# Optimization experiments

Hardware: AMD Instinct MI355X
Metric: run time of the kernel (lower is better)

The kernel has to match this reference:

```python
import jax, jax.numpy as jnp
import numpy as np
from jax.scipy.linalg import expm

B = 16384
K = 64          # number of subgroups
M = 6           # mat_dim per subgroup (subgroup_size = 36)
NUM_ACTIONS = 16


def setup_inputs() -> dict:
    key = jax.random.key(0)
    k1, k2, k3, k4 = jax.random.split(key, 4)
    group_feats = jax.random.normal(k1, (B, K * M * M), dtype=jnp.float32)
    act = jax.random.randint(k2, (B,), 0, NUM_ACTIONS)
    act_params = jax.random.normal(k3, (NUM_ACTIONS, K), dtype=jnp.float32) * 0.001
    lie_alg_basis = jax.random.normal(k4, (K, M, M), dtype=jnp.float32)
    return {"group_feats": group_feats, "act": act,
            "act_params": act_params, "lie_alg_basis": lie_alg_basis}


def reference(group_feats, act, act_params, lie_alg_basis):
    # apply_act: act_repr = blockdiag_k expm(a_{bk} * (L_k - L_k^T)); out = act_repr @ blockdiag(group_feats)
    sel = act_params[act]                                   # [B, K]  (index_select on act_params)
    skew = lie_alg_basis - jnp.swapaxes(lie_alg_basis, -2, -1)  # [K, M, M]
    lie_alg = sel[:, :, None, None] * skew[None]            # [B, K, M, M]
    # batched matrix exponential over all B*K small blocks
    lie_group = jax.vmap(expm)(lie_alg.reshape(-1, M, M)).reshape(B, K, M, M)
    gf_mat = group_feats.reshape(B, K, M, M)                # to_group_matrix (block-diag blocks)
    # block-diagonal matmul == full dense matmul since off-diagonal blocks are zero
    post = jnp.einsum('bkij,bkjl->bkil', lie_group, gf_mat)
    return post.reshape(B, K * M * M)                       # to_group_feats
```

## Files before the change

### kernel.cpp

```cpp
#include <hip/hip_runtime.h>
#include <stdint.h>

#define BATCH 16384
#define KSUB 64
#define MDIM 6
#define MM 36
#define NACT 16
#define F4PB 9
#define BLK 256
#define LDSPITCH 37

__global__ void expm_table_kernel(const float* __restrict__ act_params,
                                  const float* __restrict__ basis,
                                  float* __restrict__ Rtab)
{
    int gid = blockIdx.x * blockDim.x + threadIdx.x;
    if (gid >= NACT * KSUB) return;
    int a = gid / KSUB;
    int k = gid - a * KSUB;

    float L[MM];
#pragma unroll
    for (int i = 0; i < MM; ++i) L[i] = basis[k * MM + i];
    float p = act_params[a * KSUB + k];

    float A[MM];
#pragma unroll
    for (int i = 0; i < MDIM; ++i)
#pragma unroll
        for (int j = 0; j < MDIM; ++j)
            A[i * MDIM + j] = p * (L[i * MDIM + j] - L[j * MDIM + i]);

    float E[MM], T[MM];
#pragma unroll
    for (int i = 0; i < MM; ++i) { E[i] = 0.f; T[i] = 0.f; }
#pragma unroll
    for (int i = 0; i < MDIM; ++i) { E[i * MDIM + i] = 1.f; T[i * MDIM + i] = 1.f; }

    for (int n = 1; n <= 10; ++n) {
        float Tn[MM];
        float inv = 1.0f / (float)n;
#pragma unroll
        for (int i = 0; i < MDIM; ++i)
#pragma unroll
            for (int l = 0; l < MDIM; ++l) {
                float s = 0.f;
#pragma unroll
                for (int j = 0; j < MDIM; ++j)
                    s += A[i * MDIM + j] * T[j * MDIM + l];
                Tn[i * MDIM + l] = s * inv;
            }
#pragma unroll
        for (int i = 0; i < MM; ++i) { T[i] = Tn[i]; E[i] += Tn[i]; }
    }
#pragma unroll
    for (int i = 0; i < MM; ++i) Rtab[gid * MM + i] = E[i];
}

__global__ __launch_bounds__(BLK) void apply_kernel(
    const float4* __restrict__ gf4,
    const int* __restrict__ act,
    const float* __restrict__ Rtab,
    float4* __restrict__ out4)
{
    __shared__ float lds[BLK * LDSPITCH];
    const int tid = threadIdx.x;
    const size_t base4 = (size_t)blockIdx.x * (BLK * F4PB);

#pragma unroll
    for (int i = 0; i < F4PB; ++i) {
        int p4 = tid + i * BLK;
        float4 v = gf4[base4 + p4];
        int n = p4 / F4PB;
        int j = (p4 - n * F4PB) * 4;
        float* row = &lds[n * LDSPITCH + j];
        row[0] = v.x; row[1] = v.y; row[2] = v.z; row[3] = v.w;
    }
    __syncthreads();

    const int nblk = blockIdx.x * BLK + tid;
    const int b = nblk >> 6;
    const int k = nblk & 63;
    const int a = act[b];

    float Rv[MM];
    const float4* R4 = (const float4*)(Rtab + (a * KSUB + k) * MM);
#pragma unroll
    for (int q = 0; q < F4PB; ++q) {
        float4 v = R4[q];
        Rv[4 * q + 0] = v.x; Rv[4 * q + 1] = v.y;
        Rv[4 * q + 2] = v.z; Rv[4 * q + 3] = v.w;
    }

    float G[MM];
#pragma unroll
    for (int j = 0; j < MM; ++j) G[j] = lds[tid * LDSPITCH + j];

    float O[MM];
#pragma unroll
    for (int i = 0; i < MM; ++i) O[i] = 0.f;
#pragma unroll
    for (int j = 0; j < MDIM; ++j)
#pragma unroll
        for (int i = 0; i < MDIM; ++i) {
            float r = Rv[i * MDIM + j];
#pragma unroll
            for (int l = 0; l < MDIM; ++l)
                O[i * MDIM + l] = fmaf(r, G[j * MDIM + l], O[i * MDIM + l]);
        }

#pragma unroll
    for (int j = 0; j < MM; ++j) lds[tid * LDSPITCH + j] = O[j];
    __syncthreads();

#pragma unroll
    for (int i = 0; i < F4PB; ++i) {
        int p4 = tid + i * BLK;
        int n = p4 / F4PB;
        int j = (p4 - n * F4PB) * 4;
        const float* row = &lds[n * LDSPITCH + j];
        float4 v;
        v.x = row[0]; v.y = row[1]; v.z = row[2]; v.w = row[3];
        out4[base4 + p4] = v;
    }
}

extern "C" void kernel_launch(void* const* d_in, const int* in_sizes, int n_in,
                              void* d_out, int out_size, void* d_ws, size_t ws_size,
                              hipStream_t stream) {
    const float* gf    = (const float*)d_in[0];
    const int*   act   = (const int*)d_in[1];
    const float* ap    = (const float*)d_in[2];
    const float* basis = (const float*)d_in[3];

    float* Rtab = (float*)d_ws;

    expm_table_kernel<<<4, 256, 0, stream>>>(ap, basis, Rtab);

    const int nwg = (BATCH * KSUB) / BLK;
    apply_kernel<<<nwg, BLK, 0, stream>>>((const float4*)gf, act, Rtab,
                                          (float4*)d_out);
}
```

Baseline: 286.9 us.

## Use one-wave workgroups per batch row with nontemporal I/O and early table prefetch

Changes the apply kernel to one 64-thread workgroup per batch element, so the action lookup is a single scalar load per block. The rotation table row is prefetched into registers before the LDS staging loads, and the streaming input and output traffic uses nontemporal loads and stores to avoid polluting the cache. A barrier is added before the LDS reuse. The trade-off is 16384 small workgroups with more scheduling overhead and less LDS per block.

New measurement: 269.1 us. 6.2% less time.

```diff
diff --git a/kernel.cpp b/kernel.cpp
--- a/kernel.cpp
+++ b/kernel.cpp
@@ -7,8 +7,10 @@
 #define MM 36
 #define NACT 16
 #define F4PB 9
-#define BLK 256
+#define WGT 64
 #define LDSPITCH 37
+
+typedef float f32x4 __attribute__((ext_vector_type(4)));
 
 __global__ void expm_table_kernel(const float* __restrict__ act_params,
                                   const float* __restrict__ basis,
@@ -57,20 +59,27 @@
     for (int i = 0; i < MM; ++i) Rtab[gid * MM + i] = E[i];
 }
 
-__global__ __launch_bounds__(BLK) void apply_kernel(
-    const float4* __restrict__ gf4,
+__global__ __launch_bounds__(WGT, 4) void apply_kernel(
+    const f32x4* __restrict__ gf4,
     const int* __restrict__ act,
     const float* __restrict__ Rtab,
-    float4* __restrict__ out4)
+    f32x4* __restrict__ out4)
 {
-    __shared__ float lds[BLK * LDSPITCH];
+    __shared__ float lds[WGT * LDSPITCH];
     const int tid = threadIdx.x;
-    const size_t base4 = (size_t)blockIdx.x * (BLK * F4PB);
+    const int b = blockIdx.x;
+    const size_t base4 = (size_t)b * (WGT * F4PB);
+
+    const int a = act[b];
+    const f32x4* R4 = (const f32x4*)(Rtab + (size_t)((a << 6) + tid) * MM);
+    f32x4 rv[F4PB];
+#pragma unroll
+    for (int q = 0; q < F4PB; ++q) rv[q] = R4[q];
 
 #pragma unroll
     for (int i = 0; i < F4PB; ++i) {
-        int p4 = tid + i * BLK;
-        float4 v = gf4[base4 + p4];
+        int p4 = tid + (i << 6);
+        f32x4 v = __builtin_nontemporal_load(&gf4[base4 + p4]);
         int n = p4 / F4PB;
         int j = (p4 - n * F4PB) * 4;
         float* row = &lds[n * LDSPITCH + j];
@@ -78,24 +87,16 @@
     }
     __syncthreads();
 
-    const int nblk = blockIdx.x * BLK + tid;
-    const int b = nblk >> 6;
-    const int k = nblk & 63;
-    const int a = act[b];
-
-    float Rv[MM];
-    const float4* R4 = (const float4*)(Rtab + (a * KSUB + k) * MM);
-#pragma unroll
-    for (int q = 0; q < F4PB; ++q) {
-        float4 v = R4[q];
-        Rv[4 * q + 0] = v.x; Rv[4 * q + 1] = v.y;
-        Rv[4 * q + 2] = v.z; Rv[4 * q + 3] = v.w;
-    }
-
     float G[MM];
 #pragma unroll
     for (int j = 0; j < MM; ++j) G[j] = lds[tid * LDSPITCH + j];
 
+    float Rv[MM];
+#pragma unroll
+    for (int q = 0; q < F4PB; ++q) {
+        Rv[4 * q + 0] = rv[q].x; Rv[4 * q + 1] = rv[q].y;
+        Rv[4 * q + 2] = rv[q].z; Rv[4 * q + 3] = rv[q].w;
+    }
     float O[MM];
 #pragma unroll
     for (int i = 0; i < MM; ++i) O[i] = 0.f;
@@ -109,19 +110,20 @@
                 O[i * MDIM + l] = fmaf(r, G[j * MDIM + l], O[i * MDIM + l]);
         }
 
+    __syncthreads();
 #pragma unroll
     for (int j = 0; j < MM; ++j) lds[tid * LDSPITCH + j] = O[j];
     __syncthreads();
 
 #pragma unroll
     for (int i = 0; i < F4PB; ++i) {
-        int p4 = tid + i * BLK;
+        int p4 = tid + (i << 6);
         int n = p4 / F4PB;
         int j = (p4 - n * F4PB) * 4;
         const float* row = &lds[n * LDSPITCH + j];
-        float4 v;
+        f32x4 v;
         v.x = row[0]; v.y = row[1]; v.z = row[2]; v.w = row[3];
-        out4[base4 + p4] = v;
+        __builtin_nontemporal_store(v, &out4[base4 + p4]);
     }
 }
 
@@ -135,9 +137,8 @@
 
     float* Rtab = (float*)d_ws;
 
-    expm_table_kernel<<<4, 256, 0, stream>>>(ap, basis, Rtab);
+    expm_table_kernel<<<16, 64, 0, stream>>>(ap, basis, Rtab);
 
-    const int nwg = (BATCH * KSUB) / BLK;
-    apply_kernel<<<nwg, BLK, 0, stream>>>((const float4*)gf, act, Rtab,
-                                          (float4*)d_out);
+    apply_kernel<<<BATCH, WGT, 0, stream>>>((const f32x4*)gf, act, Rtab,
+                                            (f32x4*)d_out);
 }
```
